# Performance work log

Hardware: AMD Instinct MI355X
Metric: run time of the kernel (lower is better)

## Reference

```python
import jax, jax.numpy as jnp
import numpy as np

N_BINS = 15


def setup_inputs() -> dict:
    key = jax.random.key(0)
    k1, k2 = jax.random.split(key)
    N = 33554432  # 32Mi elements
    logits = jax.random.normal(k1, (N,), dtype=jnp.float32) * 2.0
    labels = jax.random.randint(k2, (N,), 0, 2, dtype=jnp.int32)
    return {"logits": logits, "labels": labels}


def reference(logits, labels):
    # probs = sigmoid(logits); acc = (probs > 0.5) == labels
    probs = jax.nn.sigmoid(logits)
    acc = ((probs > 0.5).astype(labels.dtype) == labels).astype(probs.dtype)

    # Bins are (lower, upper] with edges = linspace(0, 1, n_bins+1).
    # digitize(..., right=True) gives i s.t. edges[i-1] < p <= edges[i].
    edges = jnp.linspace(0.0, 1.0, N_BINS + 1)
    idx = jnp.clip(jnp.digitize(probs, edges, right=True) - 1, 0, N_BINS - 1)
    # p == 0 falls in no bin in the original loop (first bin is (0, 1/15]).
    valid = (probs > edges[0]).astype(probs.dtype)

    # ece = sum_b |mean_conf_b - mean_acc_b| * (count_b / N)
    #     = sum_b |sum_conf_b - sum_acc_b| / N   (empty bins contribute 0)
    sum_conf = jax.ops.segment_sum(probs * valid, idx, num_segments=N_BINS)
    sum_acc = jax.ops.segment_sum(acc * valid, idx, num_segments=N_BINS)
    n = jnp.asarray(probs.size, probs.dtype)
    ece = jnp.sum(jnp.abs(sum_conf - sum_acc)) / n
    return ece.reshape(1)
```

## Files before the change

### kernel.cpp

```cpp
#include <hip/hip_runtime.h>

#define NBINS 15
#define NTHREADS 256
#define NWAVES 4
#define NBLOCKS 2048

__global__ __launch_bounds__(NTHREADS) void ece_partial_kernel(
    const float* __restrict__ logits,
    const int* __restrict__ labels,
    float* __restrict__ partials,
    int n)
{
    float S[NBINS];
    #pragma unroll
    for (int k = 0; k < NBINS; ++k) S[k] = 0.0f;

    const int tid  = threadIdx.x;
    const int lane = tid & 63;
    const int w    = tid >> 6;

    const int n4 = n >> 2;
    const float4* L4 = (const float4*)logits;
    const int4*   Y4 = (const int4*)labels;
    const int stride = NBLOCKS * NTHREADS;

    for (int i = blockIdx.x * NTHREADS + tid; i < n4; i += stride) {
        float4 x = L4[i];
        int4   y = Y4[i];
        #pragma unroll
        for (int j = 0; j < 4; ++j) {
            float xv = (&x.x)[j];
            int   yv = (&y.x)[j];
            float p = 1.0f / (1.0f + __expf(-xv));
            float a = ((p > 0.5f) == (yv != 0)) ? 1.0f : 0.0f;
            float t = p - a;
            #pragma unroll
            for (int k = 0; k < NBINS; ++k) {
                const float edge = (float)k / 15.0f;
                S[k] += (p > edge) ? t : 0.0f;
            }
        }
    }

    if (blockIdx.x == 0) {
        for (int i = (n4 << 2) + tid; i < n; i += NTHREADS) {
            float xv = logits[i];
            int   yv = labels[i];
            float p = 1.0f / (1.0f + __expf(-xv));
            float a = ((p > 0.5f) == (yv != 0)) ? 1.0f : 0.0f;
            float t = p - a;
            #pragma unroll
            for (int k = 0; k < NBINS; ++k) {
                const float edge = (float)k / 15.0f;
                S[k] += (p > edge) ? t : 0.0f;
            }
        }
    }

    __shared__ float wavesum[NWAVES][NBINS];
    #pragma unroll
    for (int k = 0; k < NBINS; ++k) {
        float s = S[k];
        #pragma unroll
        for (int m = 32; m >= 1; m >>= 1)
            s += __shfl_xor(s, m, 64);
        if (lane == 0) wavesum[w][k] = s;
    }
    __syncthreads();

    if (tid < NBINS) {
        float s = 0.0f;
        #pragma unroll
        for (int ww = 0; ww < NWAVES; ++ww) s += wavesum[ww][tid];
        partials[blockIdx.x * NBINS + tid] = s;
    }
}

__global__ __launch_bounds__(NTHREADS) void ece_final_kernel(
    const float* __restrict__ partials,
    float* __restrict__ out,
    float inv_n)
{
    __shared__ double red[NBINS];
    const int t = threadIdx.x;
    if (t < 16 * NBINS) {
        const int b   = t >> 4;
        const int sub = t & 15;
        double s = 0.0;
        for (int k = sub; k < NBLOCKS; k += 16)
            s += (double)partials[k * NBINS + b];
        s += __shfl_xor(s, 8, 16);
        s += __shfl_xor(s, 4, 16);
        s += __shfl_xor(s, 2, 16);
        s += __shfl_xor(s, 1, 16);
        if (sub == 0) red[b] = s;
    }
    __syncthreads();
    if (t == 0) {
        double e = 0.0;
        #pragma unroll
        for (int b = 0; b < NBINS - 1; ++b)
            e += fabs(red[b] - red[b + 1]);
        e += fabs(red[NBINS - 1]);
        out[0] = (float)(e * (double)inv_n);
    }
}

extern "C" void kernel_launch(void* const* d_in, const int* in_sizes, int n_in,
                              void* d_out, int out_size, void* d_ws, size_t ws_size,
                              hipStream_t stream)
{
    const float* logits = (const float*)d_in[0];
    const int*   labels = (const int*)d_in[1];
    float* out      = (float*)d_out;
    float* partials = (float*)d_ws;
    const int n = in_sizes[0];

    ece_partial_kernel<<<NBLOCKS, NTHREADS, 0, stream>>>(logits, labels, partials, n);
    ece_final_kernel<<<1, NTHREADS, 0, stream>>>(partials, out, 1.0f / (float)n);
}
```

Before: 97.43 us.

## Software-pipeline loads with inline asm and compare logits against logit-space bin edges

Adds a fully unrolled path, used when n equals exactly 16 grid strides of float4s. It keeps three outstanding dwordx4 loads per thread through inline asm global_load instructions and explicit vmcnt waits, so memory latency overlaps with the per-bin accumulation. The bin tests now compare the raw logit against precomputed logit-space edges held in constant memory, which lets the comparisons run independently of the sigmoid result. This relies on the harness size matching the special case, otherwise the generic loop runs. Comparing logits near the edges may also give slightly different results than comparing sigmoid outputs.

```diff
diff --git a/kernel.cpp b/kernel.cpp
--- a/kernel.cpp
+++ b/kernel.cpp
@@ -4,6 +4,44 @@
 #define NTHREADS 256
 #define NWAVES 4
 #define NBLOCKS 2048
+#define TT (NBLOCKS * NTHREADS)
+#define ITERS 16
+
+typedef float f32x4 __attribute__((ext_vector_type(4)));
+typedef int   i32x4 __attribute__((ext_vector_type(4)));
+
+__constant__ float CEc[NBINS] = { -88.72284f,
+    -2.63905733f, -1.87180218f, -1.38629436f, -1.01160091f,
+    -0.69314718f, -0.40546511f, -0.13353139f,  0.13353139f,
+     0.40546511f,  0.69314718f,  1.01160091f,  1.38629436f,
+     1.87180218f,  2.63905733f };
+
+#define ISSUE(s) do {                                                        \
+    asm volatile("global_load_dwordx4 %0, %1, off"                           \
+                 : "=v"(xb[s]) : "v"(aL) : "memory");                        \
+    asm volatile("global_load_dwordx4 %0, %1, off"                           \
+                 : "=v"(yb[s]) : "v"(aY) : "memory");                        \
+    aL += TT; aY += TT; } while (0)
+
+#define WAITC(N) do {                                                        \
+    asm volatile("s_waitcnt vmcnt(" #N ")" ::: "memory");                    \
+    __builtin_amdgcn_sched_barrier(0); } while (0)
+
+#define COMPUTE(s) do {                                                      \
+    _Pragma("unroll")                                                        \
+    for (int j = 0; j < 4; ++j) {                                            \
+        float xv = xb[s][j];                                                 \
+        int   yv = yb[s][j];                                                 \
+        float p = 1.0f / (1.0f + __expf(-xv));                               \
+        float a = ((xv > 0.0f) == (yv != 0)) ? 1.0f : 0.0f;                  \
+        float t = p - a;                                                     \
+        _Pragma("unroll")                                                    \
+        for (int k = 0; k < NBINS; ++k)                                      \
+            S[k] += (xv > CEc[k]) ? t : 0.0f;                                \
+    } } while (0)
+
+#define STEP(s)     do { WAITC(4); COMPUTE(s); ISSUE(s); } while (0)
+#define FSTEP(s,N)  do { WAITC(N); COMPUTE(s); } while (0)
 
 __global__ __launch_bounds__(NTHREADS) void ece_partial_kernel(
     const float* __restrict__ logits,
@@ -18,41 +56,48 @@
     const int tid  = threadIdx.x;
     const int lane = tid & 63;
     const int w    = tid >> 6;
+    const int n4   = n >> 2;
 
-    const int n4 = n >> 2;
-    const float4* L4 = (const float4*)logits;
-    const int4*   Y4 = (const int4*)labels;
-    const int stride = NBLOCKS * NTHREADS;
-
-    for (int i = blockIdx.x * NTHREADS + tid; i < n4; i += stride) {
-        float4 x = L4[i];
-        int4   y = Y4[i];
-        #pragma unroll
-        for (int j = 0; j < 4; ++j) {
-            float xv = (&x.x)[j];
-            int   yv = (&y.x)[j];
-            float p = 1.0f / (1.0f + __expf(-xv));
-            float a = ((p > 0.5f) == (yv != 0)) ? 1.0f : 0.0f;
-            float t = p - a;
+    if (((n & 3) == 0) && (n4 == ITERS * TT)) {
+        const f32x4* aL = (const f32x4*)logits + (blockIdx.x * NTHREADS + tid);
+        const i32x4* aY = (const i32x4*)labels + (blockIdx.x * NTHREADS + tid);
+        f32x4 xb[3];
+        i32x4 yb[3];
+        ISSUE(0); ISSUE(1); ISSUE(2);
+        STEP(0); STEP(1); STEP(2);
+        STEP(0); STEP(1); STEP(2);
+        STEP(0); STEP(1); STEP(2);
+        STEP(0); STEP(1); STEP(2);
+        STEP(0);
+        FSTEP(1,4); FSTEP(2,2); FSTEP(0,0);
+    } else {
+        const float4* L4 = (const float4*)logits;
+        const int4*   Y4 = (const int4*)labels;
+        for (int i = blockIdx.x * NTHREADS + tid; i < n4; i += TT) {
+            float4 x = L4[i];
+            int4   y = Y4[i];
             #pragma unroll
-            for (int k = 0; k < NBINS; ++k) {
-                const float edge = (float)k / 15.0f;
-                S[k] += (p > edge) ? t : 0.0f;
+            for (int j = 0; j < 4; ++j) {
+                float xv = (&x.x)[j];
+                int   yv = (&y.x)[j];
+                float p = 1.0f / (1.0f + __expf(-xv));
+                float a = ((xv > 0.0f) == (yv != 0)) ? 1.0f : 0.0f;
+                float t = p - a;
+                #pragma unroll
+                for (int k = 0; k < NBINS; ++k)
+                    S[k] += (xv > CEc[k]) ? t : 0.0f;
             }
         }
-    }
-
-    if (blockIdx.x == 0) {
-        for (int i = (n4 << 2) + tid; i < n; i += NTHREADS) {
-            float xv = logits[i];
-            int   yv = labels[i];
-            float p = 1.0f / (1.0f + __expf(-xv));
-            float a = ((p > 0.5f) == (yv != 0)) ? 1.0f : 0.0f;
-            float t = p - a;
-            #pragma unroll
-            for (int k = 0; k < NBINS; ++k) {
-                const float edge = (float)k / 15.0f;
-                S[k] += (p > edge) ? t : 0.0f;
+        if (blockIdx.x == 0) {
+            for (int r = (n4 << 2) + tid; r < n; r += NTHREADS) {
+                float xv = logits[r];
+                int   yv = labels[r];
+                float p = 1.0f / (1.0f + __expf(-xv));
+                float a = ((xv > 0.0f) == (yv != 0)) ? 1.0f : 0.0f;
+                float t = p - a;
+                #pragma unroll
+                for (int k = 0; k < NBINS; ++k)
+                    S[k] += (xv > CEc[k]) ? t : 0.0f;
             }
         }
     }
@@ -62,8 +107,8 @@
     for (int k = 0; k < NBINS; ++k) {
         float s = S[k];
         #pragma unroll
-        for (int m = 32; m >= 1; m >>= 1)
-            s += __shfl_xor(s, m, 64);
+        for (int m2 = 32; m2 >= 1; m2 >>= 1)
+            s += __shfl_xor(s, m2, 64);
         if (lane == 0) wavesum[w][k] = s;
     }
     __syncthreads();
```

Measured after the change: 96.14 us. No clear change (-1.3%).

## Replace cumulative threshold accumulation with direct bin index and LDS atomics

Applied to the files above, without the earlier changes.

Instead of adding each element's (p - acc) into all 15 cumulative threshold sums and differencing at the end, computes the bin index via ceil(p*15) and atomically adds into per-wave shared-memory bins. Loads are unrolled 4x with nontemporal hints, and the final reduction uses 1024 threads summing |bin| directly. This cuts per-element ALU work but introduces contended LDS float atomics across 15 addresses per wave.

```diff
diff --git a/kernel.cpp b/kernel.cpp
--- a/kernel.cpp
+++ b/kernel.cpp
@@ -4,6 +4,21 @@
 #define NTHREADS 256
 #define NWAVES 4
 #define NBLOCKS 2048
+#define TT (NBLOCKS * NTHREADS)
+#define UNROLL 4
+
+typedef float f32x4 __attribute__((ext_vector_type(4)));
+typedef int   i32x4 __attribute__((ext_vector_type(4)));
+
+__device__ __forceinline__ void accum_elem(float xv, int yv, float* binrow)
+{
+    float p = 1.0f / (1.0f + __expf(-xv));
+    float a = ((xv > 0.0f) == (yv != 0)) ? 1.0f : 0.0f;
+    float t = (p > 0.0f) ? (p - a) : 0.0f;
+    int b = (int)ceilf(p * 15.0f) - 1;
+    b = min(max(b, 0), NBINS - 1);
+    atomicAdd(&binrow[b], t);
+}
 
 __global__ __launch_bounds__(NTHREADS) void ece_partial_kernel(
     const float* __restrict__ logits,
@@ -11,97 +26,84 @@
     float* __restrict__ partials,
     int n)
 {
-    float S[NBINS];
-    #pragma unroll
-    for (int k = 0; k < NBINS; ++k) S[k] = 0.0f;
-
-    const int tid  = threadIdx.x;
-    const int lane = tid & 63;
-    const int w    = tid >> 6;
+    __shared__ float bins[NWAVES][16];
+    const int tid = threadIdx.x;
+    const int w   = tid >> 6;
+    if (tid < NWAVES * 16) ((float*)bins)[tid] = 0.0f;
+    __syncthreads();
+    float* binrow = bins[w];
 
     const int n4 = n >> 2;
-    const float4* L4 = (const float4*)logits;
-    const int4*   Y4 = (const int4*)labels;
-    const int stride = NBLOCKS * NTHREADS;
+    const f32x4* L4 = (const f32x4*)logits;
+    const i32x4* Y4 = (const i32x4*)labels;
 
-    for (int i = blockIdx.x * NTHREADS + tid; i < n4; i += stride) {
-        float4 x = L4[i];
-        int4   y = Y4[i];
+    const int macroStride = TT * UNROLL;
+    const int nMacro = n4 / macroStride;
+
+    int i = blockIdx.x * (NTHREADS * UNROLL) + tid;
+    for (int m = 0; m < nMacro; ++m, i += macroStride) {
+        f32x4 x[UNROLL];
+        i32x4 y[UNROLL];
         #pragma unroll
-        for (int j = 0; j < 4; ++j) {
-            float xv = (&x.x)[j];
-            int   yv = (&y.x)[j];
-            float p = 1.0f / (1.0f + __expf(-xv));
-            float a = ((p > 0.5f) == (yv != 0)) ? 1.0f : 0.0f;
-            float t = p - a;
+        for (int u = 0; u < UNROLL; ++u) {
+            x[u] = __builtin_nontemporal_load(L4 + i + u * NTHREADS);
+            y[u] = __builtin_nontemporal_load(Y4 + i + u * NTHREADS);
+        }
+        #pragma unroll
+        for (int u = 0; u < UNROLL; ++u)
             #pragma unroll
-            for (int k = 0; k < NBINS; ++k) {
-                const float edge = (float)k / 15.0f;
-                S[k] += (p > edge) ? t : 0.0f;
-            }
-        }
+            for (int j = 0; j < 4; ++j)
+                accum_elem(x[u][j], y[u][j], binrow);
+    }
+
+    for (int r = nMacro * macroStride + blockIdx.x * NTHREADS + tid;
+         r < n4; r += TT) {
+        f32x4 x = __builtin_nontemporal_load(L4 + r);
+        i32x4 y = __builtin_nontemporal_load(Y4 + r);
+        #pragma unroll
+        for (int j = 0; j < 4; ++j)
+            accum_elem(x[j], y[j], binrow);
     }
 
     if (blockIdx.x == 0) {
-        for (int i = (n4 << 2) + tid; i < n; i += NTHREADS) {
-            float xv = logits[i];
-            int   yv = labels[i];
-            float p = 1.0f / (1.0f + __expf(-xv));
-            float a = ((p > 0.5f) == (yv != 0)) ? 1.0f : 0.0f;
-            float t = p - a;
-            #pragma unroll
-            for (int k = 0; k < NBINS; ++k) {
-                const float edge = (float)k / 15.0f;
-                S[k] += (p > edge) ? t : 0.0f;
-            }
-        }
+        for (int r = (n4 << 2) + tid; r < n; r += NTHREADS)
+            accum_elem(logits[r], labels[r], binrow);
     }
 
-    __shared__ float wavesum[NWAVES][NBINS];
-    #pragma unroll
-    for (int k = 0; k < NBINS; ++k) {
-        float s = S[k];
-        #pragma unroll
-        for (int m = 32; m >= 1; m >>= 1)
-            s += __shfl_xor(s, m, 64);
-        if (lane == 0) wavesum[w][k] = s;
-    }
     __syncthreads();
 
     if (tid < NBINS) {
         float s = 0.0f;
         #pragma unroll
-        for (int ww = 0; ww < NWAVES; ++ww) s += wavesum[ww][tid];
+        for (int ww = 0; ww < NWAVES; ++ww) s += bins[ww][tid];
         partials[blockIdx.x * NBINS + tid] = s;
     }
 }
 
-__global__ __launch_bounds__(NTHREADS) void ece_final_kernel(
+__global__ __launch_bounds__(1024) void ece_final_kernel(
     const float* __restrict__ partials,
     float* __restrict__ out,
     float inv_n)
 {
     __shared__ double red[NBINS];
     const int t = threadIdx.x;
-    if (t < 16 * NBINS) {
-        const int b   = t >> 4;
-        const int sub = t & 15;
+    if (t < 64 * NBINS) {
+        const int b   = t >> 6;
+        const int sub = t & 63;
         double s = 0.0;
-        for (int k = sub; k < NBLOCKS; k += 16)
+        for (int k = sub; k < NBLOCKS; k += 64)
             s += (double)partials[k * NBINS + b];
-        s += __shfl_xor(s, 8, 16);
-        s += __shfl_xor(s, 4, 16);
-        s += __shfl_xor(s, 2, 16);
-        s += __shfl_xor(s, 1, 16);
+        #pragma unroll
+        for (int m = 32; m >= 1; m >>= 1)
+            s += __shfl_xor(s, m, 64);
         if (sub == 0) red[b] = s;
     }
     __syncthreads();
     if (t == 0) {
         double e = 0.0;
         #pragma unroll
-        for (int b = 0; b < NBINS - 1; ++b)
-            e += fabs(red[b] - red[b + 1]);
-        e += fabs(red[NBINS - 1]);
+        for (int b = 0; b < NBINS; ++b)
+            e += fabs(red[b]);
         out[0] = (float)(e * (double)inv_n);
     }
 }
@@ -117,5 +119,5 @@
     const int n = in_sizes[0];
 
     ece_partial_kernel<<<NBLOCKS, NTHREADS, 0, stream>>>(logits, labels, partials, n);
-    ece_final_kernel<<<1, NTHREADS, 0, stream>>>(partials, out, 1.0f / (float)n);
+    ece_final_kernel<<<1, 1024, 0, stream>>>(partials, out, 1.0f / (float)n);
 }
```

Measured after the change: 189.6 us. 94.6% more time.
